# Kernel tuning notes

Measured on AMD Instinct MI355X. Metric: run time of the kernel, lower is better.

The kernel has to match this reference:

```python
import jax, jax.numpy as jnp
import numpy as np

D_HEAD = 64

def setup_inputs() -> dict:
    key = jax.random.key(0)
    kq, kk, kv, kc = jax.random.split(key, 4)
    B, H, T, D = 2, 16, 2048, D_HEAD
    Q = jax.random.normal(kq, (B, H, T, D), dtype=jnp.float32)
    K = jax.random.normal(kk, (B, H, T, D), dtype=jnp.float32)
    V = jax.random.normal(kv, (B, H, T, D), dtype=jnp.float32)
    # causal mask: True = attend
    mask = jnp.tril(jnp.ones((T, T), dtype=jnp.bool_))
    curvature = jax.random.normal(kc, (H, D, D), dtype=jnp.float32) * 0.02
    return {"Q": Q, "K": K, "V": V, "mask": mask, "curvature": curvature}

def reference(Q, K, V, mask, curvature):
    scale = 1.0 / np.sqrt(Q.shape[-1]).astype(np.float32)
    # per-head learned rotation of Q
    Q_rot = jnp.einsum('bhtd,hde->bhte', Q, curvature)
    scores = jnp.einsum('bhtd,bhsd->bhts', Q_rot, K) * scale  # [B,H,T,T]
    scores = jnp.where(mask[None, None, :, :], scores, -jnp.inf)
    attn = jax.nn.softmax(scores, axis=-1)
    out = jnp.einsum('bhts,bhsd->bhtd', attn, V)
    return out
```

## Files before the change

kernel.cpp:

```cpp
#include <hip/hip_runtime.h>


typedef __attribute__((ext_vector_type(8))) short short8;
typedef __attribute__((ext_vector_type(8))) unsigned short ushort8;
typedef __attribute__((ext_vector_type(4))) float f32x4;
typedef __attribute__((ext_vector_type(2))) _Float16 half2v;
typedef __attribute__((ext_vector_type(4))) _Float16 half4;
typedef __attribute__((ext_vector_type(8))) _Float16 half8;

constexpr int Tc = 2048;
constexpr int Dc = 64;
constexpr size_t REGION = (size_t)32 * Tc * Dc;

__device__ inline unsigned short f2bf(float f) {
    union { float f; unsigned u; } x; x.f = f;
    return (unsigned short)((x.u + 0x7fffu + ((x.u >> 16) & 1u)) >> 16);
}

__device__ inline half2v pkrtz(float a, float b) {
    return __builtin_bit_cast(half2v, __builtin_amdgcn_cvt_pkrtz(a, b));
}

#define MFMA_BF16_K32(a, b, c) __builtin_amdgcn_mfma_f32_16x16x32_bf16((a), (b), (c), 0, 0, 0)
#define MFMA_F16_K16(a, b, c)  __builtin_amdgcn_mfma_f32_16x16x16f16((a), (b), (c), 0, 0, 0)

typedef __attribute__((address_space(3))) unsigned int        lds_u32;
typedef const __attribute__((address_space(1))) unsigned int  glob_u32;
__device__ __attribute__((always_inline)) inline void gl_lds16(const void* g, void* l) {
    __builtin_amdgcn_global_load_lds((glob_u32*)g, (lds_u32*)l, 16, 0, 0);
}

__global__ __launch_bounds__(256, 1)
void holo_cfrag(const float* __restrict__ Cp, unsigned short* __restrict__ cfrag_g)
{
    const int t = threadIdx.x, lane = t & 63, eb = t >> 6;
    const int l15 = lane & 15, quad = lane >> 4;
    const int h = blockIdx.x;
    const float* Cg = Cp + (size_t)h * Dc * Dc;
    #pragma unroll
    for (int half = 0; half < 2; ++half) {
        short8 b;
        #pragma unroll
        for (int jj = 0; jj < 8; ++jj) {
            const int d = half * 32 + quad * 8 + jj;
            b[jj] = (short)f2bf(Cg[d * Dc + eb * 16 + l15]);
        }
        *(short8*)(&cfrag_g[(((size_t)h * 4 + eb) * 2 + half) * 512 + lane * 8]) = b;
    }
}

__global__ __launch_bounds__(256, 4)
void holo_prep8(const float* __restrict__ Qp, const float* __restrict__ Kp,
                const float* __restrict__ Vp,
                const unsigned short* __restrict__ cfrag_g,
                unsigned short* __restrict__ qfrag_g,
                unsigned short* __restrict__ kfrag_g,
                _Float16* __restrict__ vfrag_g)
{
    __shared__ unsigned short kt[64 * 72];
    __shared__ unsigned short qt[64 * 72];
    __shared__ _Float16      vt[64 * 72];
    __shared__ unsigned short pf[64 * 72];

    const int t = threadIdx.x, lane = t & 63, w = t >> 6;
    const int l15 = lane & 15, quad = lane >> 4, wb = w * 16;
    const int n = blockIdx.x, bh = n >> 5, st = n & 31, h = bh & 15;
    const int s0 = st * 64;

    const float* Qg = Qp + ((size_t)bh * Tc + s0) * Dc;
    const float* Kg = Kp + ((size_t)bh * Tc + s0) * Dc;
    const float* Vg = Vp + ((size_t)bh * Tc + s0) * Dc;

    #pragma unroll
    for (int kk = 0; kk < 4; ++kk) {
        const int flat = kk * 1024 + t * 4;
        const int r = flat >> 6, d0 = flat & 63;
        float4 kv = *(const float4*)(&Kg[flat]);
        ushort4 kp; kp.x = f2bf(kv.x); kp.y = f2bf(kv.y); kp.z = f2bf(kv.z); kp.w = f2bf(kv.w);
        *(ushort4*)(&kt[r * 72 + d0]) = kp;
        float4 qv = *(const float4*)(&Qg[flat]);
        ushort4 qp; qp.x = f2bf(qv.x); qp.y = f2bf(qv.y); qp.z = f2bf(qv.z); qp.w = f2bf(qv.w);
        *(ushort4*)(&qt[r * 72 + d0]) = qp;
        float4 vv = *(const float4*)(&Vg[flat]);
        half4 vp;
        vp[0] = (_Float16)vv.x; vp[1] = (_Float16)vv.y;
        vp[2] = (_Float16)vv.z; vp[3] = (_Float16)vv.w;
        *(half4*)(&vt[r * 72 + d0]) = vp;
    }
    __syncthreads();

    {
        const int row = wb + l15;
        ushort8 p0 = *(const ushort8*)(&kt[row * 72 + quad * 8]);
        ushort8 p1 = *(const ushort8*)(&kt[row * 72 + 32 + quad * 8]);
        unsigned short* ktile = kfrag_g + (size_t)(bh * 32 + st) * 4096;
        *(ushort8*)(&ktile[(w * 64 + lane) * 8])        = p0;
        *(ushort8*)(&ktile[2048 + (w * 64 + lane) * 8]) = p1;
    }

    {
        half8 v0, v1;
        #pragma unroll
        for (int dn = 0; dn < 2; ++dn)
            #pragma unroll
            for (int i = 0; i < 4; ++i)
                v0[dn * 4 + i] = vt[(wb + quad * 4 + i) * 72 + dn * 16 + l15];
        #pragma unroll
        for (int dn = 0; dn < 2; ++dn)
            #pragma unroll
            for (int i = 0; i < 4; ++i)
                v1[dn * 4 + i] = vt[(wb + quad * 4 + i) * 72 + (dn + 2) * 16 + l15];
        _Float16* vtile = vfrag_g + (size_t)(bh * 32 + st) * 4096;
        *(half8*)(&vtile[(w * 64 + lane) * 8])        = v0;
        *(half8*)(&vtile[2048 + (w * 64 + lane) * 8]) = v1;
    }

    {
        short8 a0 = *(const short8*)(&qt[(wb + l15) * 72 + quad * 8]);
        short8 a1 = *(const short8*)(&qt[(wb + l15) * 72 + 32 + quad * 8]);
        #pragma unroll
        for (int eb = 0; eb < 4; ++eb) {
            short8 b0 = *(const short8*)(&cfrag_g[(((size_t)h * 4 + eb) * 2 + 0) * 512 + lane * 8]);
            short8 b1 = *(const short8*)(&cfrag_g[(((size_t)h * 4 + eb) * 2 + 1) * 512 + lane * 8]);
            f32x4 c = {0.f, 0.f, 0.f, 0.f};
            c = MFMA_BF16_K32(a0, b0, c);
            c = MFMA_BF16_K32(a1, b1, c);
            #pragma unroll
            for (int i = 0; i < 4; ++i)
                pf[(wb + quad * 4 + i) * 72 + eb * 16 + l15] = f2bf(c[i] * 0.18033688f);
        }
        __threadfence_block();
        short8 fa0 = *(const short8*)(&pf[(wb + l15) * 72 + quad * 8]);
        short8 fa1 = *(const short8*)(&pf[(wb + l15) * 72 + 32 + quad * 8]);
        const size_t strip = (size_t)bh * 128 + st * 4 + w;
        *(short8*)(&qfrag_g[strip * 1024 + lane * 8]) = fa0;
        *(short8*)(&qfrag_g[strip * 1024 + 512 + lane * 8]) = fa1;
    }
}

__global__ __launch_bounds__(256, 4)
void holo_attn19(const unsigned short* __restrict__ qfrag_g,
                 const unsigned short* __restrict__ kfrag_g,
                 const _Float16* __restrict__ vfrag_g,
                 float* __restrict__ Op)
{
    __shared__ unsigned short bufK[2][4096];
    __shared__ _Float16      bufV[2][4096];

    const int t = threadIdx.x, lane = t & 63, wid = t >> 6;
    const int l15 = lane & 15, quad = lane >> 4;

    const int id = blockIdx.x;
    const int xcd = id & 7, sseq = id >> 3;
    const int qi = 31 - (sseq >> 2);
    const int bh = xcd * 4 + (sseq & 3);
    const int q0 = qi * 64;

    const char* kbase = (const char*)(kfrag_g + (size_t)bh * 32 * 4096);
    const char* vbase = (const char*)(vfrag_g + (size_t)bh * 32 * 4096);

    {
        gl_lds16(kbase + wid * 1024 + lane * 16,        &bufK[0][wid * 512]);
        gl_lds16(kbase + 4096 + wid * 1024 + lane * 16, &bufK[0][2048 + wid * 512]);
        gl_lds16(vbase + wid * 1024 + lane * 16,        &bufV[0][wid * 512]);
        gl_lds16(vbase + 4096 + wid * 1024 + lane * 16, &bufV[0][2048 + wid * 512]);
    }

    short8 qa0, qa1;
    {
        const size_t strip = (size_t)bh * 128 + qi * 4 + wid;
        qa0 = *(const short8*)(&qfrag_g[strip * 1024 + lane * 8]);
        qa1 = *(const short8*)(&qfrag_g[strip * 1024 + 512 + lane * 8]);
    }

    f32x4 o[4];
    #pragma unroll
    for (int dn = 0; dn < 4; ++dn) o[dn] = f32x4{0.f, 0.f, 0.f, 0.f};
    float l_lane = 0.f;
    const int rowg = q0 + wid * 16 + l15;

    asm volatile("s_waitcnt vmcnt(0)" ::: "memory");
    __builtin_amdgcn_sched_barrier(0);
    __syncthreads();

    int cur = 0;
    for (int j = 0; j <= qi; ++j) {
        if (j < qi) {
            const char* ks = kbase + (size_t)(j + 1) * 8192;
            const char* vs = vbase + (size_t)(j + 1) * 8192;
            const int nb = cur ^ 1;
            gl_lds16(ks + wid * 1024 + lane * 16,        &bufK[nb][wid * 512]);
            gl_lds16(ks + 4096 + wid * 1024 + lane * 16, &bufK[nb][2048 + wid * 512]);
            gl_lds16(vs + wid * 1024 + lane * 16,        &bufV[nb][wid * 512]);
            gl_lds16(vs + 4096 + wid * 1024 + lane * 16, &bufV[nb][2048 + wid * 512]);
        }

        const unsigned short* Kl = &bufK[cur][0];
        const _Float16*       Vl = &bufV[cur][0];

        f32x4 st[4];
        __builtin_amdgcn_s_setprio(1);
        #pragma unroll
        for (int tn = 0; tn < 4; ++tn) {
            short8 k0 = *(const short8*)(&Kl[(tn * 64 + lane) * 8]);
            short8 k1 = *(const short8*)(&Kl[2048 + (tn * 64 + lane) * 8]);
            f32x4 c = {0.f, 0.f, 0.f, 0.f};
            c = MFMA_BF16_K32(k0, qa0, c);
            c = MFMA_BF16_K32(k1, qa1, c);
            st[tn] = c;
        }
        __builtin_amdgcn_s_setprio(0);

        half4 pa[4];
        #pragma unroll
        for (int tn = 0; tn < 4; ++tn) {
            float p[4];
            #pragma unroll
            for (int i = 0; i < 4; ++i) {
                float sv = st[tn][i];
                if (j == qi) {
                    const int colg = j * 64 + tn * 16 + quad * 4 + i;
                    if (colg > rowg) sv = -1e30f;
                }
                p[i] = __builtin_amdgcn_exp2f(sv);
                l_lane += p[i];
            }
            half2v lo = pkrtz(p[0], p[1]), hi = pkrtz(p[2], p[3]);
            pa[tn] = __builtin_shufflevector(lo, hi, 0, 1, 2, 3);
        }

        __builtin_amdgcn_s_setprio(1);
        #pragma unroll
        for (int tn = 0; tn < 4; ++tn) {
            half8 vl = *(const half8*)(&Vl[(tn * 64 + lane) * 8]);
            half8 vh = *(const half8*)(&Vl[2048 + (tn * 64 + lane) * 8]);
            half4 vf0 = __builtin_shufflevector(vl, vl, 0, 1, 2, 3);
            half4 vf1 = __builtin_shufflevector(vl, vl, 4, 5, 6, 7);
            half4 vf2 = __builtin_shufflevector(vh, vh, 0, 1, 2, 3);
            half4 vf3 = __builtin_shufflevector(vh, vh, 4, 5, 6, 7);
            o[0] = MFMA_F16_K16(vf0, pa[tn], o[0]);
            o[1] = MFMA_F16_K16(vf1, pa[tn], o[1]);
            o[2] = MFMA_F16_K16(vf2, pa[tn], o[2]);
            o[3] = MFMA_F16_K16(vf3, pa[tn], o[3]);
        }
        __builtin_amdgcn_s_setprio(0);

        asm volatile("s_waitcnt vmcnt(0)" ::: "memory");
        __builtin_amdgcn_sched_barrier(0);
        __syncthreads();
        cur ^= 1;
    }

    l_lane += __shfl_xor(l_lane, 16);
    l_lane += __shfl_xor(l_lane, 32);
    const float inv = 1.0f / l_lane;

    float* dst = Op + ((size_t)bh * Tc + rowg) * Dc;
    #pragma unroll
    for (int dn = 0; dn < 4; ++dn) {
        float4 r;
        r.x = o[dn][0] * inv; r.y = o[dn][1] * inv;
        r.z = o[dn][2] * inv; r.w = o[dn][3] * inv;
        *(float4*)(&dst[dn * 16 + quad * 4]) = r;
    }
}

extern "C" void kernel_launch(void* const* d_in, const int* in_sizes, int n_in,
                              void* d_out, int out_size, void* d_ws, size_t ws_size,
                              hipStream_t stream) {
    const float* Q = (const float*)d_in[0];
    const float* K = (const float*)d_in[1];
    const float* V = (const float*)d_in[2];
    const float* C = (const float*)d_in[4];
    float* O = (float*)d_out;

    unsigned short* qfrag_w = (unsigned short*)d_ws;
    unsigned short* kfrag_w = qfrag_w + REGION;
    _Float16*       vfrag_w = (_Float16*)(kfrag_w + REGION);
    unsigned short* cfrag_w = (unsigned short*)(vfrag_w + REGION);

    holo_cfrag<<<dim3(16), dim3(256), 0, stream>>>(C, cfrag_w);
    holo_prep8<<<dim3(1024), dim3(256), 0, stream>>>(Q, K, V, cfrag_w, qfrag_w, kfrag_w, vfrag_w);
    holo_attn19<<<dim3(1024), dim3(256), 0, stream>>>(qfrag_w, kfrag_w, vfrag_w, O);
}
```

Baseline: 137.5 us.

## Triple-buffer K/V tiles in LDS with partial vmcnt waits

Replaces the double-buffered K/V LDS pipeline with a three-stage ring, prefetching up to three tiles ahead. Each iteration waits only for the oldest outstanding loads (vmcnt 8/4/0) instead of draining all memory ops, and the refill is issued after a barrier. This is meant to hide more global-load latency. In exchange, LDS use per block grows by half and launch bounds drop from 4 to 3 blocks per CU, which may reduce occupancy.

After: 136.2 us. Within noise of the previous version (-1.0%).

```diff
diff --git a/kernel.cpp b/kernel.cpp
--- a/kernel.cpp
+++ b/kernel.cpp
@@ -138,14 +138,14 @@
     }
 }
 
-__global__ __launch_bounds__(256, 4)
-void holo_attn19(const unsigned short* __restrict__ qfrag_g,
+__global__ __launch_bounds__(256, 3)
+void holo_attn21(const unsigned short* __restrict__ qfrag_g,
                  const unsigned short* __restrict__ kfrag_g,
                  const _Float16* __restrict__ vfrag_g,
                  float* __restrict__ Op)
 {
-    __shared__ unsigned short bufK[2][4096];
-    __shared__ _Float16      bufV[2][4096];
+    __shared__ unsigned short bufK[3][4096];
+    __shared__ _Float16      bufV[3][4096];
 
     const int t = threadIdx.x, lane = t & 63, wid = t >> 6;
     const int l15 = lane & 15, quad = lane >> 4;
@@ -159,19 +159,24 @@
     const char* kbase = (const char*)(kfrag_g + (size_t)bh * 32 * 4096);
     const char* vbase = (const char*)(vfrag_g + (size_t)bh * 32 * 4096);
 
-    {
-        gl_lds16(kbase + wid * 1024 + lane * 16,        &bufK[0][wid * 512]);
-        gl_lds16(kbase + 4096 + wid * 1024 + lane * 16, &bufK[0][2048 + wid * 512]);
-        gl_lds16(vbase + wid * 1024 + lane * 16,        &bufV[0][wid * 512]);
-        gl_lds16(vbase + 4096 + wid * 1024 + lane * 16, &bufV[0][2048 + wid * 512]);
-    }
-
     short8 qa0, qa1;
     {
         const size_t strip = (size_t)bh * 128 + qi * 4 + wid;
         qa0 = *(const short8*)(&qfrag_g[strip * 1024 + lane * 8]);
         qa1 = *(const short8*)(&qfrag_g[strip * 1024 + 512 + lane * 8]);
     }
+    asm volatile("s_waitcnt vmcnt(0)" ::: "memory");
+    __builtin_amdgcn_sched_barrier(0);
+
+    const int npre = (qi + 1 < 3) ? qi + 1 : 3;
+    for (int p = 0; p < npre; ++p) {
+        const char* ks = kbase + (size_t)p * 8192;
+        const char* vs = vbase + (size_t)p * 8192;
+        gl_lds16(ks + wid * 1024 + lane * 16,        &bufK[p][wid * 512]);
+        gl_lds16(ks + 4096 + wid * 1024 + lane * 16, &bufK[p][2048 + wid * 512]);
+        gl_lds16(vs + wid * 1024 + lane * 16,        &bufV[p][wid * 512]);
+        gl_lds16(vs + 4096 + wid * 1024 + lane * 16, &bufV[p][2048 + wid * 512]);
+    }
 
     f32x4 o[4];
     #pragma unroll
@@ -179,24 +184,19 @@
     float l_lane = 0.f;
     const int rowg = q0 + wid * 16 + l15;
 
-    asm volatile("s_waitcnt vmcnt(0)" ::: "memory");
-    __builtin_amdgcn_sched_barrier(0);
-    __syncthreads();
-
-    int cur = 0;
+    int fly = npre;
+    int cs  = 0;
+
     for (int j = 0; j <= qi; ++j) {
-        if (j < qi) {
-            const char* ks = kbase + (size_t)(j + 1) * 8192;
-            const char* vs = vbase + (size_t)(j + 1) * 8192;
-            const int nb = cur ^ 1;
-            gl_lds16(ks + wid * 1024 + lane * 16,        &bufK[nb][wid * 512]);
-            gl_lds16(ks + 4096 + wid * 1024 + lane * 16, &bufK[nb][2048 + wid * 512]);
-            gl_lds16(vs + wid * 1024 + lane * 16,        &bufV[nb][wid * 512]);
-            gl_lds16(vs + 4096 + wid * 1024 + lane * 16, &bufV[nb][2048 + wid * 512]);
-        }
-
-        const unsigned short* Kl = &bufK[cur][0];
-        const _Float16*       Vl = &bufV[cur][0];
+        if (fly == 3)      { asm volatile("s_waitcnt vmcnt(8)" ::: "memory"); }
+        else if (fly == 2) { asm volatile("s_waitcnt vmcnt(4)" ::: "memory"); }
+        else               { asm volatile("s_waitcnt vmcnt(0)" ::: "memory"); }
+        __builtin_amdgcn_sched_barrier(0);
+        __builtin_amdgcn_s_barrier();
+        __builtin_amdgcn_sched_barrier(0);
+
+        const unsigned short* Kl = &bufK[cs][0];
+        const _Float16*       Vl = &bufV[cs][0];
 
         f32x4 st[4];
         __builtin_amdgcn_s_setprio(1);
@@ -245,10 +245,20 @@
         }
         __builtin_amdgcn_s_setprio(0);
 
-        asm volatile("s_waitcnt vmcnt(0)" ::: "memory");
-        __builtin_amdgcn_sched_barrier(0);
-        __syncthreads();
-        cur ^= 1;
+        __builtin_amdgcn_sched_barrier(0);
+        __builtin_amdgcn_s_barrier();
+        __builtin_amdgcn_sched_barrier(0);
+        if (j + 3 <= qi) {
+            const char* ks = kbase + (size_t)(j + 3) * 8192;
+            const char* vs = vbase + (size_t)(j + 3) * 8192;
+            gl_lds16(ks + wid * 1024 + lane * 16,        &bufK[cs][wid * 512]);
+            gl_lds16(ks + 4096 + wid * 1024 + lane * 16, &bufK[cs][2048 + wid * 512]);
+            gl_lds16(vs + wid * 1024 + lane * 16,        &bufV[cs][wid * 512]);
+            gl_lds16(vs + 4096 + wid * 1024 + lane * 16, &bufV[cs][2048 + wid * 512]);
+        } else {
+            --fly;
+        }
+        cs = (cs == 2) ? 0 : cs + 1;
     }
 
     l_lane += __shfl_xor(l_lane, 16);
@@ -281,5 +291,5 @@
 
     holo_cfrag<<<dim3(16), dim3(256), 0, stream>>>(C, cfrag_w);
     holo_prep8<<<dim3(1024), dim3(256), 0, stream>>>(Q, K, V, cfrag_w, qfrag_w, kfrag_w, vfrag_w);
-    holo_attn19<<<dim3(1024), dim3(256), 0, stream>>>(qfrag_w, kfrag_w, vfrag_w, O);
-}
+    holo_attn21<<<dim3(1024), dim3(256), 0, stream>>>(qfrag_w, kfrag_w, vfrag_w, O);
+}
```
